# Kernel tuning notes

Measured on AMD Instinct MI355X. Metric: run time of the kernel, lower is better.

## Reference

```python
import jax, jax.numpy as jnp
import numpy as np

NUM_STATES = 512
NUM_OBS = 1024
BATCH = 64
T = 512


def setup_inputs() -> dict:
    key = jax.random.key(0)
    k_obs, k_pi, k_A, k_B = jax.random.split(key, 4)
    observations = jax.random.randint(k_obs, (BATCH, T), 0, NUM_OBS, dtype=jnp.int32)
    log_pi = jax.random.normal(k_pi, (NUM_STATES,), dtype=jnp.float32)
    log_A = jax.random.normal(k_A, (NUM_STATES, NUM_STATES), dtype=jnp.float32)
    log_B = jax.random.normal(k_B, (NUM_STATES, NUM_OBS), dtype=jnp.float32)
    return {"observations": observations, "log_pi": log_pi, "log_A": log_A, "log_B": log_B}


def _hmm_loglik(observations, log_pi, log_A, log_B):
    # Normalize parameters in log-space (as in the torch module).
    lpi = jax.nn.log_softmax(log_pi, axis=0)            # (S,)
    lA = jax.nn.log_softmax(log_A, axis=1)              # (S, S)
    lB = jax.nn.log_softmax(log_B, axis=1)              # (S, O)

    # Emission log-probs per timestep: (B, T, S)
    emit = lB.T[observations]                            # gather columns of lB

    alpha0 = lpi[None, :] + emit[:, 0, :]                # (B, S)

    def step(alpha, emit_t):
        # alpha: (B, S) over previous state i; transition lA[i, j]
        alpha_next = jax.scipy.special.logsumexp(alpha[:, :, None] + lA[None, :, :], axis=1) + emit_t
        return alpha_next, None

    # scan over time axis; emit[:, 1:, :] -> (T-1, B, S)
    alpha_T, _ = jax.lax.scan(step, alpha0, jnp.swapaxes(emit[:, 1:, :], 0, 1))
    log_probs = jax.scipy.special.logsumexp(alpha_T, axis=1)  # (B,)
    return log_probs.sum()


def reference(observations, log_pi, log_A, log_B):
    return _hmm_loglik(observations, log_pi, log_A, log_B)
```

## Files before the change

kernel.cpp:

```cpp
#include <hip/hip_runtime.h>

#define S     512
#define NOBS  1024
#define TT    512
#define CH    16
#define NWAVE 8
#define NJT   4
#define NGRP  4

typedef __attribute__((ext_vector_type(4))) float f32x4;
typedef __attribute__((ext_vector_type(4))) int   i32x4;
typedef __attribute__((ext_vector_type(8))) int   i32x8;
typedef __attribute__((ext_vector_type(2))) unsigned int u32x2;
typedef long i64;

__device__ __forceinline__ unsigned short f2bf(float x) {
  unsigned u = __builtin_bit_cast(unsigned, x);
  return (unsigned short)((u + 0x7fffu + ((u >> 16) & 1u)) >> 16);
}
__device__ __forceinline__ float bflo(unsigned u) {
  return __builtin_bit_cast(float, u << 16);
}
__device__ __forceinline__ float bfhi_raw(unsigned u) {
  return __builtin_bit_cast(float, u);
}
__device__ __forceinline__ float bfhi(unsigned u) {
  return __builtin_bit_cast(float, u & 0xffff0000u);
}

__device__ __forceinline__ unsigned char f2fp8_sw(float x) {
  x = fminf(fmaxf(x, 0.f), 448.f);
  unsigned u = __builtin_bit_cast(unsigned, x);
  int ex = (int)((u >> 23) & 0xff);
  if (ex >= 121) {
    unsigned m = (u & 0x7fffff) | 0x800000;
    unsigned keep = m >> 20, rest = m & 0xfffff;
    keep += (rest > 0x80000u) || (rest == 0x80000u && (keep & 1));
    int e8 = ex - 127 + 7;
    if (keep == 16) { keep = 8; e8++; }
    if (e8 >= 16) return 0x7e;
    return (unsigned char)((e8 << 3) | (keep & 7));
  } else {
    int m = (int)(x * 512.0f + 0.5f);
    if (m > 8) m = 8;
    return (unsigned char)m;
  }
}

__device__ __forceinline__ unsigned pack4_fp8(float p0, float p1, float p2, float p3) {
#if __has_builtin(__builtin_amdgcn_cvt_pk_fp8_f32)
  int v = __builtin_amdgcn_cvt_pk_fp8_f32(p0, p1, 0, false);
  v = __builtin_amdgcn_cvt_pk_fp8_f32(p2, p3, v, true);
  return (unsigned)v;
#else
  return (unsigned)f2fp8_sw(p0) | ((unsigned)f2fp8_sw(p1) << 8) |
         ((unsigned)f2fp8_sw(p2) << 16) | ((unsigned)f2fp8_sw(p3) << 24);
#endif
}

__device__ __forceinline__ float wave_max(float v) {
  for (int d = 32; d; d >>= 1) v = fmaxf(v, __shfl_xor(v, d));
  return v;
}
__device__ __forceinline__ float wave_sum(float v) {
  for (int d = 32; d; d >>= 1) v += __shfl_xor(v, d);
  return v;
}

__global__ void prep_pi(const float* __restrict__ log_pi, float* __restrict__ lpi) {
  const int l = threadIdx.x;
  float v[8];
  float mx = -INFINITY;
  for (int k = 0; k < 8; ++k) { v[k] = log_pi[l + 64 * k]; mx = fmaxf(mx, v[k]); }
  mx = wave_max(mx);
  float sm = 0.f;
  for (int k = 0; k < 8; ++k) sm += __expf(v[k] - mx);
  sm = wave_sum(sm);
  const float lse = mx + __logf(sm);
  for (int k = 0; k < 8; ++k) lpi[l + 64 * k] = v[k] - lse;
}

__global__ void prep_B(const float* __restrict__ log_B, unsigned short* __restrict__ Bexp16) {
  const int j = blockIdx.x, l = threadIdx.x;
  const float* row = log_B + (size_t)j * NOBS;
  float v[16];
  float mx = -INFINITY;
  for (int k = 0; k < 16; ++k) { v[k] = row[l + 64 * k]; mx = fmaxf(mx, v[k]); }
  mx = wave_max(mx);
  float sm = 0.f;
  for (int k = 0; k < 16; ++k) sm += __expf(v[k] - mx);
  sm = wave_sum(sm);
  const float lse = mx + __logf(sm);
  for (int k = 0; k < 16; ++k) Bexp16[(size_t)(l + 64 * k) * S + j] = f2bf(__expf(v[k] - lse));
}

__global__ void prep_A(const float* __restrict__ log_A, unsigned char* __restrict__ Afrag8) {
  const int i = blockIdx.x, l = threadIdx.x;
  const float* row = log_A + (size_t)i * S;
  float v[8];
  float mx = -INFINITY;
  for (int k = 0; k < 8; ++k) { v[k] = row[l + 64 * k]; mx = fmaxf(mx, v[k]); }
  mx = wave_max(mx);
  float sm = 0.f;
  for (int k = 0; k < 8; ++k) sm += __expf(v[k] - mx);
  sm = wave_sum(sm);
  const float lse = mx + __logf(sm);
  const int c = i >> 7, g4s = (i >> 5) & 3, e = i & 31;
  for (int k = 0; k < 8; ++k) {
    const int j = l + 64 * k;
    const int jt = j >> 4, jc = j & 15;
    Afrag8[((size_t)(jt * 4 + c) * 64 + g4s * 16 + jc) * 32 + e] = f2fp8_sw(__expf(v[k] - lse));
  }
}

__device__ __forceinline__ int pswz(int m, int g) { return m * 512 + (((g ^ m) & 31) << 4); }

__device__ __forceinline__ float max8(const float* p) {
  const f32x4 p0 = *reinterpret_cast<const f32x4*>(p);
  const f32x4 p1 = *reinterpret_cast<const f32x4*>(p + 4);
  return fmaxf(fmaxf(fmaxf(p0[0], p0[1]), fmaxf(p0[2], p0[3])),
               fmaxf(fmaxf(p1[0], p1[1]), fmaxf(p1[2], p1[3])));
}
__device__ __forceinline__ float sum8(const float* p) {
  const f32x4 p0 = *reinterpret_cast<const f32x4*>(p);
  const f32x4 p1 = *reinterpret_cast<const f32x4*>(p + 4);
  return ((p0[0] + p0[1]) + (p0[2] + p0[3])) + ((p1[0] + p1[1]) + (p1[2] + p1[3]));
}

__device__ __forceinline__ f32x4 mfma_chunk(const i32x8 a, const i32x8 b, f32x4 acc) {
#if __has_builtin(__builtin_amdgcn_mfma_scale_f32_16x16x128_f8f6f4)
  return __builtin_amdgcn_mfma_scale_f32_16x16x128_f8f6f4(
             a, b, acc, 0, 0, 0, 0x7f7f7f7f, 0, 0x7f7f7f7f);
#else
  const i64* pa = reinterpret_cast<const i64*>(&a);
  const i64* pb = reinterpret_cast<const i64*>(&b);
  #pragma unroll
  for (int q = 0; q < 4; ++q)
    acc = __builtin_amdgcn_mfma_f32_16x16x32_fp8_fp8(pa[q], pb[q], acc, 0, 0, 0);
  return acc;
#endif
}

__global__ __launch_bounds__(512, 2)
void hmm_main(const int* __restrict__ obs, const float* __restrict__ lpi,
              const unsigned short* __restrict__ Bexp16,
              const unsigned char* __restrict__ Afrag8, float* __restrict__ parts)
{
  __shared__ __align__(16) unsigned char Pb[2][CH * S];
  __shared__ int obs_s[CH][TT + 1];
  __shared__ __align__(16) float pred[2][CH][12];

  const int tid = threadIdx.x;
  const int w = tid >> 6, l = tid & 63, g4 = l >> 4, mm = l & 15;
  const int grp = blockIdx.x;

  i32x8 a_frags[NJT][4];
  #pragma unroll
  for (int ji = 0; ji < NJT; ++ji) {
    const int jt = w + NWAVE * ji;
    #pragma unroll
    for (int cc = 0; cc < 4; ++cc) {
      const int c = (cc + w) & 3;
      a_frags[ji][cc] = *reinterpret_cast<const i32x8*>(
          Afrag8 + ((size_t)(jt * 4 + c) * 64 + l) * 32);
    }
  }

  int rd[4][2], wr[NJT];
  #pragma unroll
  for (int cc = 0; cc < 4; ++cc) {
    const int g0 = ((cc + w) & 3) * 8 + g4 * 2;
    rd[cc][0] = pswz(mm, g0);
    rd[cc][1] = pswz(mm, g0 + 1);
  }
  #pragma unroll
  for (int ji = 0; ji < NJT; ++ji) wr[ji] = pswz(mm, w + NWAVE * ji) + g4 * 4;

  for (int m = 0; m < CH; ++m)
    obs_s[m][tid] = obs[(size_t)(grp * CH + m) * TT + tid];
  __syncthreads();

  float lsc_f;
  int   lsc_i = 0;
  float Lp, e1p;

  {
    const int o0 = obs_s[mm][0];
    f32x4 vals[NJT];
    #pragma unroll
    for (int ji = 0; ji < NJT; ++ji) {
      const int j0 = (w + NWAVE * ji) * 16 + g4 * 4;
      const f32x4 lp = *reinterpret_cast<const f32x4*>(lpi + j0);
      const u32x2 e = *reinterpret_cast<const u32x2*>(Bexp16 + (size_t)o0 * S + j0);
      vals[ji][0] = lp[0] + __logf(bflo(e[0]));
      vals[ji][1] = lp[1] + __logf(bfhi(e[0]));
      vals[ji][2] = lp[2] + __logf(bflo(e[1]));
      vals[ji][3] = lp[3] + __logf(bfhi(e[1]));
    }
    float v = -INFINITY;
    #pragma unroll
    for (int ji = 0; ji < NJT; ++ji)
      v = fmaxf(v, fmaxf(fmaxf(vals[ji][0], vals[ji][1]), fmaxf(vals[ji][2], vals[ji][3])));
    v = fmaxf(v, __shfl_xor(v, 16));
    v = fmaxf(v, __shfl_xor(v, 32));
    if (g4 == 0) pred[0][mm][w] = v;
    __syncthreads();
    const float M0 = max8(&pred[0][mm][0]);
    #pragma unroll
    for (int ji = 0; ji < NJT; ++ji)
      *reinterpret_cast<unsigned*>(&Pb[0][wr[ji]]) =
          pack4_fp8(__expf(vals[ji][0] - M0), __expf(vals[ji][1] - M0),
                    __expf(vals[ji][2] - M0), __expf(vals[ji][3] - M0));
    lsc_f = M0;
    __syncthreads();
  }

  {
    const int o1 = obs_s[mm][1];
    u32x2 eb[NJT];
    const unsigned short* bp = Bexp16 + ((size_t)o1 << 9) + g4 * 4 + w * 16;
    #pragma unroll
    for (int ji = 0; ji < NJT; ++ji)
      eb[ji] = *reinterpret_cast<const u32x2*>(bp + ji * 128);

    f32x4 acc[NJT];
    #pragma unroll
    for (int ji = 0; ji < NJT; ++ji) acc[ji] = f32x4{0.f, 0.f, 0.f, 0.f};
    #pragma unroll
    for (int cc = 0; cc < 4; ++cc) {
      i32x8 af;
      i32x4* h = reinterpret_cast<i32x4*>(&af);
      h[0] = *reinterpret_cast<const i32x4*>(&Pb[0][rd[cc][0]]);
      h[1] = *reinterpret_cast<const i32x4*>(&Pb[0][rd[cc][1]]);
      #pragma unroll
      for (int ji = 0; ji < NJT; ++ji)
        acc[ji] = mfma_chunk(a_frags[ji][cc], af, acc[ji]);
    }
    f32x4 vals[NJT];
    #pragma unroll
    for (int ji = 0; ji < NJT; ++ji) {
      vals[ji][0] = acc[ji][0] * bflo(eb[ji][0]);
      vals[ji][1] = acc[ji][1] * bfhi(eb[ji][0]);
      vals[ji][2] = acc[ji][2] * bflo(eb[ji][1]);
      vals[ji][3] = acc[ji][3] * bfhi(eb[ji][1]);
    }
    float v = -INFINITY;
    #pragma unroll
    for (int ji = 0; ji < NJT; ++ji)
      v = fmaxf(v, fmaxf(fmaxf(vals[ji][0], vals[ji][1]), fmaxf(vals[ji][2], vals[ji][3])));
    v = fmaxf(v, __shfl_xor(v, 16));
    v = fmaxf(v, __shfl_xor(v, 32));
    if (g4 == 0) pred[1][mm][w] = v;
    __syncthreads();
    const float v1 = max8(&pred[1][mm][0]);
    const float inv = __builtin_amdgcn_rcpf(v1);
    lsc_f += __logf(v1);
    Lp = __log2f(v1); e1p = 0.f;
    #pragma unroll
    for (int ji = 0; ji < NJT; ++ji)
      *reinterpret_cast<unsigned*>(&Pb[1][wr[ji]]) =
          pack4_fp8(vals[ji][0] * inv, vals[ji][1] * inv,
                    vals[ji][2] * inv, vals[ji][3] * inv);
    __syncthreads();
  }

  for (int t = 2; t < TT - 1; ++t) {
    const int cur = t & 1;
    const unsigned char* __restrict__ pprv = Pb[cur ^ 1];
    unsigned char* __restrict__ pcur = Pb[cur];

    const int ob = obs_s[mm][t];
    u32x2 eb[NJT];
    const unsigned short* bp = Bexp16 + ((size_t)ob << 9) + g4 * 4 + w * 16;
    #pragma unroll
    for (int ji = 0; ji < NJT; ++ji)
      eb[ji] = *reinterpret_cast<const u32x2*>(bp + ji * 128);

    const float pm = max8(&pred[cur ^ 1][mm][0]);

    f32x4 acc[NJT];
    #pragma unroll
    for (int ji = 0; ji < NJT; ++ji) acc[ji] = f32x4{0.f, 0.f, 0.f, 0.f};
    #pragma unroll
    for (int cc = 0; cc < 4; ++cc) {
      i32x8 af;
      i32x4* h = reinterpret_cast<i32x4*>(&af);
      h[0] = *reinterpret_cast<const i32x4*>(pprv + rd[cc][0]);
      h[1] = *reinterpret_cast<const i32x4*>(pprv + rd[cc][1]);
      #pragma unroll
      for (int ji = 0; ji < NJT; ++ji)
        acc[ji] = mfma_chunk(a_frags[ji][cc], af, acc[ji]);
    }

    const float e_new = (t == 2) ? 0.f : __log2f(pm);
    const float dsr = fminf(fmaxf(e_new - e1p, -3.0f), 3.0f);
    int s = (int)__builtin_rintf(Lp + e_new + dsr);
    s = min(max(s, -60), 60);
    Lp = (float)s; e1p = e_new; lsc_i += s;
    const float pw2 = __builtin_bit_cast(float, (unsigned)(127 - s) << 23);

    float vmax = 0.f;
    #pragma unroll
    for (int ji = 0; ji < NJT; ++ji) {
      const float q0 = acc[ji][0] * (bflo(eb[ji][0]) * pw2);
      const float q1 = acc[ji][1] * (bfhi_raw(eb[ji][0]) * pw2);
      const float q2 = acc[ji][2] * (bflo(eb[ji][1]) * pw2);
      const float q3 = acc[ji][3] * (bfhi_raw(eb[ji][1]) * pw2);
      *reinterpret_cast<unsigned*>(pcur + wr[ji]) = pack4_fp8(q0, q1, q2, q3);
      vmax = fmaxf(fmaxf(vmax, fmaxf(fmaxf(q0, q1), q2)), q3);
    }
    vmax = fmaxf(vmax, __shfl_xor(vmax, 16));
    vmax = fmaxf(vmax, __shfl_xor(vmax, 32));
    if (g4 == 0) pred[cur][mm][w] = vmax;
    __syncthreads();
  }

  {
    const int t = TT - 1, cur = t & 1;
    const unsigned char* __restrict__ pprv = Pb[cur ^ 1];
    const int ob = obs_s[mm][t];
    u32x2 eb[NJT];
    const unsigned short* bp = Bexp16 + ((size_t)ob << 9) + g4 * 4 + w * 16;
    #pragma unroll
    for (int ji = 0; ji < NJT; ++ji)
      eb[ji] = *reinterpret_cast<const u32x2*>(bp + ji * 128);
    const float pm = max8(&pred[cur ^ 1][mm][0]);

    f32x4 acc[NJT];
    #pragma unroll
    for (int ji = 0; ji < NJT; ++ji) acc[ji] = f32x4{0.f, 0.f, 0.f, 0.f};
    #pragma unroll
    for (int cc = 0; cc < 4; ++cc) {
      i32x8 af;
      i32x4* h = reinterpret_cast<i32x4*>(&af);
      h[0] = *reinterpret_cast<const i32x4*>(pprv + rd[cc][0]);
      h[1] = *reinterpret_cast<const i32x4*>(pprv + rd[cc][1]);
      #pragma unroll
      for (int ji = 0; ji < NJT; ++ji)
        acc[ji] = mfma_chunk(a_frags[ji][cc], af, acc[ji]);
    }

    const float e_new = __log2f(pm);
    const float dsr = fminf(fmaxf(e_new - e1p, -3.0f), 3.0f);
    int s = (int)__builtin_rintf(Lp + e_new + dsr);
    s = min(max(s, -60), 60);
    lsc_i += s;
    const float pw2 = __builtin_bit_cast(float, (unsigned)(127 - s) << 23);

    float ssum = 0.f;
    #pragma unroll
    for (int ji = 0; ji < NJT; ++ji)
      ssum += acc[ji][0] * bflo(eb[ji][0]) + acc[ji][1] * bfhi(eb[ji][0]) +
              acc[ji][2] * bflo(eb[ji][1]) + acc[ji][3] * bfhi(eb[ji][1]);
    ssum *= pw2;
    ssum += __shfl_xor(ssum, 16);
    ssum += __shfl_xor(ssum, 32);
    if (g4 == 0) pred[cur][mm][w] = ssum;
    __syncthreads();
    if (w == 0 && g4 == 0) {
      const float s8 = sum8(&pred[cur][mm][0]);
      float cl = lsc_f + (float)lsc_i * 0.69314718056f + __logf(s8);
      for (int d = 1; d < 16; d <<= 1) cl += __shfl_xor(cl, d);
      if (l == 0) parts[grp] = cl;
    }
  }
}

__global__ void final_sum(const float* __restrict__ parts, float* __restrict__ out) {
  out[0] = parts[0] + parts[1] + parts[2] + parts[3];
}

extern "C" void kernel_launch(void* const* d_in, const int* in_sizes, int n_in,
                              void* d_out, int out_size, void* d_ws, size_t ws_size,
                              hipStream_t stream) {
  const int*   obs  = (const int*)d_in[0];
  const float* lgpi = (const float*)d_in[1];
  const float* lgA  = (const float*)d_in[2];
  const float* lgB  = (const float*)d_in[3];
  float* out = (float*)d_out;

  char* ws = (char*)d_ws;
  unsigned short* Bexp16 = (unsigned short*)ws;
  unsigned char*  Afrag8 = (unsigned char*)(ws + (size_t)NOBS * S * 2);
  float*          lpi    = (float*)(ws + (size_t)NOBS * S * 2 + (size_t)S * S);
  float*          parts  = lpi + S;

  prep_pi<<<1, 64, 0, stream>>>(lgpi, lpi);
  prep_B<<<S, 64, 0, stream>>>(lgB, Bexp16);
  prep_A<<<S, 64, 0, stream>>>(lgA, Afrag8);
  hmm_main<<<NGRP, 512, 0, stream>>>(obs, lpi, Bexp16, Afrag8, parts);
  final_sum<<<1, 1, 0, stream>>>(parts, out);
}
```

Baseline: 701.2 us.

## Software-pipeline the HMM recurrence by overlapping each step's epilogue with next-step MFMA chunks

The time loop is restructured so the scale-and-pack epilogue of step t is split into four column tiles. Each tile is followed by a barrier and then the MFMA chunk of step t+1 that consumes exactly those rows, with accumulators and emission registers double-buffered across a two-step unrolled loop. The next step's emission loads are issued earlier, during the epilogue. This is meant to hide MFMA and epilogue latency on the serial recurrence. The cost is four block barriers per step instead of one, and the per-wave rotation of chunk order is dropped, which may bring back LDS bank contention.

```diff
diff --git a/kernel.cpp b/kernel.cpp
--- a/kernel.cpp
+++ b/kernel.cpp
@@ -141,6 +141,66 @@
 #endif
 }
 
+#define EPI_TILE(JI, ACCP, EB, PW2, PCUR, VMAX) {                                \
+  const float q0 = ACCP[JI][0] * (bflo(EB[JI][0]) * (PW2));                      \
+  const float q1 = ACCP[JI][1] * (bfhi_raw(EB[JI][0]) * (PW2));                  \
+  const float q2 = ACCP[JI][2] * (bflo(EB[JI][1]) * (PW2));                      \
+  const float q3 = ACCP[JI][3] * (bfhi_raw(EB[JI][1]) * (PW2));                  \
+  *reinterpret_cast<unsigned*>((PCUR) + wr[JI]) = pack4_fp8(q0, q1, q2, q3);     \
+  VMAX = fmaxf(fmaxf(VMAX, fmaxf(fmaxf(q0, q1), q2)), q3);                       \
+}
+
+#define MFMA_CHUNK_ACC(C, ACCN, PCUR, FIRST) {                                   \
+  i32x8 af;                                                                      \
+  i32x4* h = reinterpret_cast<i32x4*>(&af);                                      \
+  h[0] = *reinterpret_cast<const i32x4*>((PCUR) + rd[C][0]);                     \
+  h[1] = *reinterpret_cast<const i32x4*>((PCUR) + rd[C][1]);                     \
+  _Pragma("unroll")                                                              \
+  for (int ji_ = 0; ji_ < NJT; ++ji_)                                            \
+    ACCN[ji_] = mfma_chunk(a_frags[ji_][C], af,                                  \
+                           (FIRST) ? f32x4{0.f, 0.f, 0.f, 0.f} : ACCN[ji_]);     \
+}
+
+#define PREFETCH_EB(EB, T1) {                                                    \
+  const int ob_ = obs_s[mm][T1];                                                 \
+  const unsigned short* bp_ = Bexp16 + ((size_t)ob_ << 9) + g4 * 4 + w * 16;     \
+  _Pragma("unroll")                                                              \
+  for (int ji_ = 0; ji_ < NJT; ++ji_)                                            \
+    EB[ji_] = *reinterpret_cast<const u32x2*>(bp_ + ji_ * 128);                  \
+}
+
+#define STEADY_BODY(T, ACCP, ACCN, EBA, EBB) {                                   \
+  unsigned char* __restrict__ pcur = Pb[(T) & 1];                                \
+                                        \
+  const float pm_ = max8(&pred[((T) - 1) & 1][mm][0]);                           \
+  const float en_ = ((T) == 2) ? 0.f : __log2f(pm_);                             \
+  const float dr_ = fminf(fmaxf(en_ - e1p, -3.0f), 3.0f);                        \
+  int s_ = (int)__builtin_rintf(Lp + en_ + dr_);                                 \
+  s_ = min(max(s_, -60), 60);                                                    \
+  Lp = (float)s_; e1p = en_; lsc_i += s_;                                        \
+  const float pw2_ = __builtin_bit_cast(float, (unsigned)(127 - s_) << 23);      \
+  float vmax_ = 0.f;                                                             \
+  EPI_TILE(0, ACCP, EBA, pw2_, pcur, vmax_);                                     \
+  __syncthreads();                                                               \
+  MFMA_CHUNK_ACC(0, ACCN, pcur, true);                                           \
+                                                                    \
+  EPI_TILE(1, ACCP, EBA, pw2_, pcur, vmax_);                                     \
+  __syncthreads();                                                               \
+  MFMA_CHUNK_ACC(1, ACCN, pcur, false);                                          \
+                                                                    \
+  EPI_TILE(2, ACCP, EBA, pw2_, pcur, vmax_);                                     \
+  __syncthreads();                                                               \
+  PREFETCH_EB(EBB, (T) + 1);                                                     \
+  MFMA_CHUNK_ACC(2, ACCN, pcur, false);                                          \
+                                                                    \
+  EPI_TILE(3, ACCP, EBA, pw2_, pcur, vmax_);                                     \
+  vmax_ = fmaxf(vmax_, __shfl_xor(vmax_, 16));                                   \
+  vmax_ = fmaxf(vmax_, __shfl_xor(vmax_, 32));                                   \
+  if (g4 == 0) pred[(T) & 1][mm][w] = vmax_;                                     \
+  __syncthreads();                                                               \
+  MFMA_CHUNK_ACC(3, ACCN, pcur, false);                                          \
+}
+
 __global__ __launch_bounds__(512, 2)
 void hmm_main(const int* __restrict__ obs, const float* __restrict__ lpi,
               const unsigned short* __restrict__ Bexp16,
@@ -159,19 +219,17 @@
   for (int ji = 0; ji < NJT; ++ji) {
     const int jt = w + NWAVE * ji;
     #pragma unroll
-    for (int cc = 0; cc < 4; ++cc) {
-      const int c = (cc + w) & 3;
-      a_frags[ji][cc] = *reinterpret_cast<const i32x8*>(
+    for (int c = 0; c < 4; ++c)
+      a_frags[ji][c] = *reinterpret_cast<const i32x8*>(
           Afrag8 + ((size_t)(jt * 4 + c) * 64 + l) * 32);
-    }
   }
 
   int rd[4][2], wr[NJT];
   #pragma unroll
-  for (int cc = 0; cc < 4; ++cc) {
-    const int g0 = ((cc + w) & 3) * 8 + g4 * 2;
-    rd[cc][0] = pswz(mm, g0);
-    rd[cc][1] = pswz(mm, g0 + 1);
+  for (int c = 0; c < 4; ++c) {
+    const int g0 = c * 8 + g4 * 2;
+    rd[c][0] = pswz(mm, g0);
+    rd[c][1] = pswz(mm, g0 + 1);
   }
   #pragma unroll
   for (int ji = 0; ji < NJT; ++ji) wr[ji] = pswz(mm, w + NWAVE * ji) + g4 * 4;
@@ -217,32 +275,25 @@
 
   {
     const int o1 = obs_s[mm][1];
-    u32x2 eb[NJT];
+    u32x2 eb1[NJT];
     const unsigned short* bp = Bexp16 + ((size_t)o1 << 9) + g4 * 4 + w * 16;
     #pragma unroll
     for (int ji = 0; ji < NJT; ++ji)
-      eb[ji] = *reinterpret_cast<const u32x2*>(bp + ji * 128);
+      eb1[ji] = *reinterpret_cast<const u32x2*>(bp + ji * 128);
 
     f32x4 acc[NJT];
-    #pragma unroll
-    for (int ji = 0; ji < NJT; ++ji) acc[ji] = f32x4{0.f, 0.f, 0.f, 0.f};
-    #pragma unroll
-    for (int cc = 0; cc < 4; ++cc) {
-      i32x8 af;
-      i32x4* h = reinterpret_cast<i32x4*>(&af);
-      h[0] = *reinterpret_cast<const i32x4*>(&Pb[0][rd[cc][0]]);
-      h[1] = *reinterpret_cast<const i32x4*>(&Pb[0][rd[cc][1]]);
-      #pragma unroll
-      for (int ji = 0; ji < NJT; ++ji)
-        acc[ji] = mfma_chunk(a_frags[ji][cc], af, acc[ji]);
-    }
+    MFMA_CHUNK_ACC(0, acc, Pb[0], true);
+    MFMA_CHUNK_ACC(1, acc, Pb[0], false);
+    MFMA_CHUNK_ACC(2, acc, Pb[0], false);
+    MFMA_CHUNK_ACC(3, acc, Pb[0], false);
+
     f32x4 vals[NJT];
     #pragma unroll
     for (int ji = 0; ji < NJT; ++ji) {
-      vals[ji][0] = acc[ji][0] * bflo(eb[ji][0]);
-      vals[ji][1] = acc[ji][1] * bfhi(eb[ji][0]);
-      vals[ji][2] = acc[ji][2] * bflo(eb[ji][1]);
-      vals[ji][3] = acc[ji][3] * bfhi(eb[ji][1]);
+      vals[ji][0] = acc[ji][0] * bflo(eb1[ji][0]);
+      vals[ji][1] = acc[ji][1] * bfhi(eb1[ji][0]);
+      vals[ji][2] = acc[ji][2] * bflo(eb1[ji][1]);
+      vals[ji][3] = acc[ji][3] * bfhi(eb1[ji][1]);
     }
     float v = -INFINITY;
     #pragma unroll
@@ -264,82 +315,22 @@
     __syncthreads();
   }
 
-  for (int t = 2; t < TT - 1; ++t) {
-    const int cur = t & 1;
-    const unsigned char* __restrict__ pprv = Pb[cur ^ 1];
-    unsigned char* __restrict__ pcur = Pb[cur];
-
-    const int ob = obs_s[mm][t];
-    u32x2 eb[NJT];
-    const unsigned short* bp = Bexp16 + ((size_t)ob << 9) + g4 * 4 + w * 16;
-    #pragma unroll
-    for (int ji = 0; ji < NJT; ++ji)
-      eb[ji] = *reinterpret_cast<const u32x2*>(bp + ji * 128);
-
-    const float pm = max8(&pred[cur ^ 1][mm][0]);
-
-    f32x4 acc[NJT];
-    #pragma unroll
-    for (int ji = 0; ji < NJT; ++ji) acc[ji] = f32x4{0.f, 0.f, 0.f, 0.f};
-    #pragma unroll
-    for (int cc = 0; cc < 4; ++cc) {
-      i32x8 af;
-      i32x4* h = reinterpret_cast<i32x4*>(&af);
-      h[0] = *reinterpret_cast<const i32x4*>(pprv + rd[cc][0]);
-      h[1] = *reinterpret_cast<const i32x4*>(pprv + rd[cc][1]);
-      #pragma unroll
-      for (int ji = 0; ji < NJT; ++ji)
-        acc[ji] = mfma_chunk(a_frags[ji][cc], af, acc[ji]);
-    }
-
-    const float e_new = (t == 2) ? 0.f : __log2f(pm);
-    const float dsr = fminf(fmaxf(e_new - e1p, -3.0f), 3.0f);
-    int s = (int)__builtin_rintf(Lp + e_new + dsr);
-    s = min(max(s, -60), 60);
-    Lp = (float)s; e1p = e_new; lsc_i += s;
-    const float pw2 = __builtin_bit_cast(float, (unsigned)(127 - s) << 23);
-
-    float vmax = 0.f;
-    #pragma unroll
-    for (int ji = 0; ji < NJT; ++ji) {
-      const float q0 = acc[ji][0] * (bflo(eb[ji][0]) * pw2);
-      const float q1 = acc[ji][1] * (bfhi_raw(eb[ji][0]) * pw2);
-      const float q2 = acc[ji][2] * (bflo(eb[ji][1]) * pw2);
-      const float q3 = acc[ji][3] * (bfhi_raw(eb[ji][1]) * pw2);
-      *reinterpret_cast<unsigned*>(pcur + wr[ji]) = pack4_fp8(q0, q1, q2, q3);
-      vmax = fmaxf(fmaxf(vmax, fmaxf(fmaxf(q0, q1), q2)), q3);
-    }
-    vmax = fmaxf(vmax, __shfl_xor(vmax, 16));
-    vmax = fmaxf(vmax, __shfl_xor(vmax, 32));
-    if (g4 == 0) pred[cur][mm][w] = vmax;
-    __syncthreads();
-  }
+  f32x4 accA[NJT], accB[NJT];
+  u32x2 ebA[NJT], ebB[NJT];
+  PREFETCH_EB(ebA, 2);
+  MFMA_CHUNK_ACC(0, accA, Pb[1], true);
+  MFMA_CHUNK_ACC(1, accA, Pb[1], false);
+  MFMA_CHUNK_ACC(2, accA, Pb[1], false);
+  MFMA_CHUNK_ACC(3, accA, Pb[1], false);
+
+  for (int t = 2; t < 510; t += 2) {
+    STEADY_BODY(t,     accA, accB, ebA, ebB);
+    STEADY_BODY(t + 1, accB, accA, ebB, ebA);
+  }
+  STEADY_BODY(510, accA, accB, ebA, ebB);
 
   {
-    const int t = TT - 1, cur = t & 1;
-    const unsigned char* __restrict__ pprv = Pb[cur ^ 1];
-    const int ob = obs_s[mm][t];
-    u32x2 eb[NJT];
-    const unsigned short* bp = Bexp16 + ((size_t)ob << 9) + g4 * 4 + w * 16;
-    #pragma unroll
-    for (int ji = 0; ji < NJT; ++ji)
-      eb[ji] = *reinterpret_cast<const u32x2*>(bp + ji * 128);
-    const float pm = max8(&pred[cur ^ 1][mm][0]);
-
-    f32x4 acc[NJT];
-    #pragma unroll
-    for (int ji = 0; ji < NJT; ++ji) acc[ji] = f32x4{0.f, 0.f, 0.f, 0.f};
-    #pragma unroll
-    for (int cc = 0; cc < 4; ++cc) {
-      i32x8 af;
-      i32x4* h = reinterpret_cast<i32x4*>(&af);
-      h[0] = *reinterpret_cast<const i32x4*>(pprv + rd[cc][0]);
-      h[1] = *reinterpret_cast<const i32x4*>(pprv + rd[cc][1]);
-      #pragma unroll
-      for (int ji = 0; ji < NJT; ++ji)
-        acc[ji] = mfma_chunk(a_frags[ji][cc], af, acc[ji]);
-    }
-
+    const float pm = max8(&pred[0][mm][0]);
     const float e_new = __log2f(pm);
     const float dsr = fminf(fmaxf(e_new - e1p, -3.0f), 3.0f);
     int s = (int)__builtin_rintf(Lp + e_new + dsr);
@@ -350,15 +341,15 @@
     float ssum = 0.f;
     #pragma unroll
     for (int ji = 0; ji < NJT; ++ji)
-      ssum += acc[ji][0] * bflo(eb[ji][0]) + acc[ji][1] * bfhi(eb[ji][0]) +
-              acc[ji][2] * bflo(eb[ji][1]) + acc[ji][3] * bfhi(eb[ji][1]);
+      ssum += accB[ji][0] * bflo(ebB[ji][0]) + accB[ji][1] * bfhi(ebB[ji][0]) +
+              accB[ji][2] * bflo(ebB[ji][1]) + accB[ji][3] * bfhi(ebB[ji][1]);
     ssum *= pw2;
     ssum += __shfl_xor(ssum, 16);
     ssum += __shfl_xor(ssum, 32);
-    if (g4 == 0) pred[cur][mm][w] = ssum;
+    if (g4 == 0) pred[1][mm][w] = ssum;
     __syncthreads();
     if (w == 0 && g4 == 0) {
-      const float s8 = sum8(&pred[cur][mm][0]);
+      const float s8 = sum8(&pred[1][mm][0]);
       float cl = lsc_f + (float)lsc_i * 0.69314718056f + __logf(s8);
       for (int d = 1; d < 16; d <<= 1) cl += __shfl_xor(cl, d);
       if (l == 0) parts[grp] = cl;
```

New measurement: 707.6 us. No clear change (+0.9%).

## Split batch across 16 workgroups with 4 sequences each instead of 4×16

Applied to the files above, without the earlier changes.

Reduces the number of batch sequences handled per workgroup from 16 to 4 and raises the grid from 4 to 16 workgroups, so more CUs run the sequential recursion in parallel. The MFMA tiles stay 16-wide, so lanes 4-15 of each column group compute redundant padding work and are masked off from shared-memory writes. Each workgroup still loads the full transition fragments, which adds global traffic, and most MFMA throughput is wasted. The final sum now loops over NGRP partials.

```diff
diff --git a/kernel.cpp b/kernel.cpp
--- a/kernel.cpp
+++ b/kernel.cpp
@@ -3,10 +3,10 @@
 #define S     512
 #define NOBS  1024
 #define TT    512
-#define CH    16
+#define CH_V  4
 #define NWAVE 8
 #define NJT   4
-#define NGRP  4
+#define NGRP  16
 
 typedef __attribute__((ext_vector_type(4))) float f32x4;
 typedef __attribute__((ext_vector_type(4))) int   i32x4;
@@ -146,12 +146,14 @@
               const unsigned short* __restrict__ Bexp16,
               const unsigned char* __restrict__ Afrag8, float* __restrict__ parts)
 {
-  __shared__ __align__(16) unsigned char Pb[2][CH * S];
-  __shared__ int obs_s[CH][TT + 1];
-  __shared__ __align__(16) float pred[2][CH][12];
+  __shared__ __align__(16) unsigned char Pb[2][CH_V * S];
+  __shared__ int obs_s[CH_V][TT + 1];
+  __shared__ __align__(16) float pred[2][CH_V][12];
 
   const int tid = threadIdx.x;
-  const int w = tid >> 6, l = tid & 63, g4 = l >> 4, mm = l & 15;
+  const int w = tid >> 6, l = tid & 63, g4 = l >> 4;
+  const int mm = l & 3;
+  const bool wlane = ((l & 15) < CH_V);
   const int grp = blockIdx.x;
 
   i32x8 a_frags[NJT][4];
@@ -176,8 +178,9 @@
   #pragma unroll
   for (int ji = 0; ji < NJT; ++ji) wr[ji] = pswz(mm, w + NWAVE * ji) + g4 * 4;
 
-  for (int m = 0; m < CH; ++m)
-    obs_s[m][tid] = obs[(size_t)(grp * CH + m) * TT + tid];
+  #pragma unroll
+  for (int m = 0; m < CH_V; ++m)
+    obs_s[m][tid] = obs[(size_t)(grp * CH_V + m) * TT + tid];
   __syncthreads();
 
   float lsc_f;
@@ -203,14 +206,15 @@
       v = fmaxf(v, fmaxf(fmaxf(vals[ji][0], vals[ji][1]), fmaxf(vals[ji][2], vals[ji][3])));
     v = fmaxf(v, __shfl_xor(v, 16));
     v = fmaxf(v, __shfl_xor(v, 32));
-    if (g4 == 0) pred[0][mm][w] = v;
+    if (g4 == 0 && wlane) pred[0][mm][w] = v;
     __syncthreads();
     const float M0 = max8(&pred[0][mm][0]);
     #pragma unroll
     for (int ji = 0; ji < NJT; ++ji)
-      *reinterpret_cast<unsigned*>(&Pb[0][wr[ji]]) =
-          pack4_fp8(__expf(vals[ji][0] - M0), __expf(vals[ji][1] - M0),
-                    __expf(vals[ji][2] - M0), __expf(vals[ji][3] - M0));
+      if (wlane)
+        *reinterpret_cast<unsigned*>(&Pb[0][wr[ji]]) =
+            pack4_fp8(__expf(vals[ji][0] - M0), __expf(vals[ji][1] - M0),
+                      __expf(vals[ji][2] - M0), __expf(vals[ji][3] - M0));
     lsc_f = M0;
     __syncthreads();
   }
@@ -250,7 +254,7 @@
       v = fmaxf(v, fmaxf(fmaxf(vals[ji][0], vals[ji][1]), fmaxf(vals[ji][2], vals[ji][3])));
     v = fmaxf(v, __shfl_xor(v, 16));
     v = fmaxf(v, __shfl_xor(v, 32));
-    if (g4 == 0) pred[1][mm][w] = v;
+    if (g4 == 0 && wlane) pred[1][mm][w] = v;
     __syncthreads();
     const float v1 = max8(&pred[1][mm][0]);
     const float inv = __builtin_amdgcn_rcpf(v1);
@@ -258,9 +262,10 @@
     Lp = __log2f(v1); e1p = 0.f;
     #pragma unroll
     for (int ji = 0; ji < NJT; ++ji)
-      *reinterpret_cast<unsigned*>(&Pb[1][wr[ji]]) =
-          pack4_fp8(vals[ji][0] * inv, vals[ji][1] * inv,
-                    vals[ji][2] * inv, vals[ji][3] * inv);
+      if (wlane)
+        *reinterpret_cast<unsigned*>(&Pb[1][wr[ji]]) =
+            pack4_fp8(vals[ji][0] * inv, vals[ji][1] * inv,
+                      vals[ji][2] * inv, vals[ji][3] * inv);
     __syncthreads();
   }
 
@@ -306,12 +311,13 @@
       const float q1 = acc[ji][1] * (bfhi_raw(eb[ji][0]) * pw2);
       const float q2 = acc[ji][2] * (bflo(eb[ji][1]) * pw2);
       const float q3 = acc[ji][3] * (bfhi_raw(eb[ji][1]) * pw2);
-      *reinterpret_cast<unsigned*>(pcur + wr[ji]) = pack4_fp8(q0, q1, q2, q3);
+      if (wlane)
+        *reinterpret_cast<unsigned*>(pcur + wr[ji]) = pack4_fp8(q0, q1, q2, q3);
       vmax = fmaxf(fmaxf(vmax, fmaxf(fmaxf(q0, q1), q2)), q3);
     }
     vmax = fmaxf(vmax, __shfl_xor(vmax, 16));
     vmax = fmaxf(vmax, __shfl_xor(vmax, 32));
-    if (g4 == 0) pred[cur][mm][w] = vmax;
+    if (g4 == 0 && wlane) pred[cur][mm][w] = vmax;
     __syncthreads();
   }
 
@@ -355,19 +361,21 @@
     ssum *= pw2;
     ssum += __shfl_xor(ssum, 16);
     ssum += __shfl_xor(ssum, 32);
-    if (g4 == 0) pred[cur][mm][w] = ssum;
-    __syncthreads();
-    if (w == 0 && g4 == 0) {
+    if (g4 == 0 && wlane) pred[cur][mm][w] = ssum;
+    __syncthreads();
+    if (w == 0 && g4 == 0 && wlane) {
       const float s8 = sum8(&pred[cur][mm][0]);
       float cl = lsc_f + (float)lsc_i * 0.69314718056f + __logf(s8);
-      for (int d = 1; d < 16; d <<= 1) cl += __shfl_xor(cl, d);
+      for (int d = 1; d < CH_V; d <<= 1) cl += __shfl_xor(cl, d);
       if (l == 0) parts[grp] = cl;
     }
   }
 }
 
 __global__ void final_sum(const float* __restrict__ parts, float* __restrict__ out) {
-  out[0] = parts[0] + parts[1] + parts[2] + parts[3];
+  float s = 0.f;
+  for (int i = 0; i < NGRP; ++i) s += parts[i];
+  out[0] = s;
 }
 
 extern "C" void kernel_launch(void* const* d_in, const int* in_sizes, int n_in,
```

After: 784.8 us. 1.12x slower.
